# Kernel optimization log

Measured on AMD Instinct MI355X. Metric: run time of the kernel, lower is better.

Reference implementation:

```python
import jax, jax.numpy as jnp
import numpy as np

B, T, HID, NH = 2, 2048, 1024, 16
HD = HID // NH  # head_dim = 64
ROPE_BASE = 1000000.0


def _precompute_freqs(dim, end, rope_base):
    inv = 1.0 / (rope_base ** (np.arange(0, dim, 2)[: dim // 2].astype(np.float32) / dim))
    t = np.arange(end, dtype=np.float32)
    freqs = np.outer(t, inv).astype(np.float32)  # (end, dim//2)
    cos = np.concatenate([np.cos(freqs), np.cos(freqs)], axis=-1)
    sin = np.concatenate([np.sin(freqs), np.sin(freqs)], axis=-1)
    return jnp.asarray(cos), jnp.asarray(sin)


def setup_inputs() -> dict:
    key = jax.random.key(0)
    ks = jax.random.split(key, 5)
    x = jax.random.normal(ks[0], (B, T, HID), dtype=jnp.float32)
    s = 1.0 / np.sqrt(HID)
    Wq = jax.random.normal(ks[1], (HID, HID), dtype=jnp.float32) * s
    Wk = jax.random.normal(ks[2], (HID, HID), dtype=jnp.float32) * s
    Wv = jax.random.normal(ks[3], (HID, HID), dtype=jnp.float32) * s
    Wo = jax.random.normal(ks[4], (HID, HID), dtype=jnp.float32) * s
    cos, sin = _precompute_freqs(HD, T, ROPE_BASE)
    return {"x": x, "Wq": Wq, "Wk": Wk, "Wv": Wv, "Wo": Wo, "cos": cos, "sin": sin}


def _rotate_half(u):
    half = u.shape[-1] // 2
    return jnp.concatenate([-u[..., half:], u[..., :half]], axis=-1)


def reference(x, Wq, Wk, Wv, Wo, cos, sin):
    b, t, _ = x.shape
    # projections (nn.Linear: x @ W.T)
    q = (x @ Wq.T).reshape(b, t, NH, HD).transpose(0, 2, 1, 3)  # (B,H,T,D)
    k = (x @ Wk.T).reshape(b, t, NH, HD).transpose(0, 2, 1, 3)
    v = (x @ Wv.T).reshape(b, t, NH, HD).transpose(0, 2, 1, 3)
    c = cos[None, None, :t, :]
    s = sin[None, None, :t, :]
    q = q * c + _rotate_half(q) * s
    k = k * c + _rotate_half(k) * s
    scores = jnp.einsum("bhqd,bhkd->bhqk", q, k) / jnp.sqrt(jnp.float32(HD))
    causal = jnp.tril(jnp.ones((t, t), dtype=bool))
    scores = jnp.where(causal[None, None], scores, jnp.float32(-jnp.inf))
    prob = jax.nn.softmax(scores, axis=-1)
    out = jnp.einsum("bhqk,bhkd->bhqd", prob, v)
    out = out.transpose(0, 2, 1, 3).reshape(b, t, HID)
    return out @ Wo.T
```

## Files before the change

kernel.cpp:

```cpp
#include <hip/hip_runtime.h>
#include <hip/hip_bf16.h>

#define B_   2
#define T_   2048
#define HID_ 1024
#define NH_  16
#define HD_  64
#define K_   1024
#define M_   (B_*T_)

typedef __attribute__((ext_vector_type(8)))  short bf16x8;
typedef __attribute__((ext_vector_type(4)))  float f32x4;
typedef __attribute__((ext_vector_type(16))) float f32x16;
typedef __attribute__((ext_vector_type(4)))  unsigned int u32x4;

#define LOG2E 1.44269504088896340736f

__device__ inline unsigned short f2bf(float f) {
    __hip_bfloat16 h = __float2bfloat16(f);
    return __builtin_bit_cast(unsigned short, h);
}
__device__ inline float bf2f(unsigned short u) {
    return __builtin_bit_cast(float, (unsigned int)u << 16);
}
__device__ inline unsigned int pk2(float a, float b) {
    return (unsigned int)f2bf(a) | ((unsigned int)f2bf(b) << 16);
}
__device__ inline bf16x8 cvt8(float4 a, float4 b) {
    bf16x8 r;
    r[0]=(short)f2bf(a.x); r[1]=(short)f2bf(a.y); r[2]=(short)f2bf(a.z); r[3]=(short)f2bf(a.w);
    r[4]=(short)f2bf(b.x); r[5]=(short)f2bf(b.y); r[6]=(short)f2bf(b.z); r[7]=(short)f2bf(b.w);
    return r;
}

__global__ __launch_bounds__(256)
void cast_x(const float* __restrict__ in, unsigned short* __restrict__ out) {
    const int i = blockIdx.x * 256 + threadIdx.x;
    float4 a = ((const float4*)in)[2*i], b = ((const float4*)in)[2*i + 1];
    ((bf16x8*)out)[i] = cvt8(a, b);
}
__global__ __launch_bounds__(256)
void cast_w(const float* __restrict__ W0, const float* __restrict__ W1,
            const float* __restrict__ W2, const float* __restrict__ W3,
            unsigned short* __restrict__ o0, unsigned short* __restrict__ o1,
            unsigned short* __restrict__ o2, unsigned short* __restrict__ o3) {
    const int blk = blockIdx.x, sec = blk >> 9;
    const float* in = (sec == 0) ? W0 : (sec == 1) ? W1 : (sec == 2) ? W2 : W3;
    unsigned short* out = (sec == 0) ? o0 : (sec == 1) ? o1 : (sec == 2) ? o2 : o3;
    const int i = (blk & 511) * 256 + threadIdx.x;
    float4 a = ((const float4*)in)[2*i], b = ((const float4*)in)[2*i + 1];
    ((bf16x8*)out)[i] = cvt8(a, b);
}

template<int TYPE>
__global__ __launch_bounds__(256)
void gemm_k(const unsigned short* __restrict__ A, const unsigned short* __restrict__ W0,
            const unsigned short* __restrict__ W1, const unsigned short* __restrict__ W2,
            const float* __restrict__ cs, const float* __restrict__ sn,
            unsigned short* __restrict__ qb, unsigned short* __restrict__ kb,
            unsigned short* __restrict__ vtb, float* __restrict__ fout) {
    __shared__ unsigned short As[128*64];
    __shared__ unsigned short Bs[128*64];
    const int tid = threadIdx.x;
    const int w = tid >> 6, lane = tid & 63;
    const int u = lane >> 4, c = lane & 15;
    const int bm = blockIdx.x * 128, bn = blockIdx.y * 128;
    const int wm = (w & 1) * 64, wn = (w >> 1) * 64;
    const int srow = tid >> 3, scol = (tid & 7) << 3;

    const unsigned short* Wsec;
    int wrowbase;
    if constexpr (TYPE == 0) {
        const int sec = bn >> 10;
        Wsec = (sec == 0) ? W0 : ((sec == 1) ? W1 : W2);
        wrowbase = bn & 1023;
    } else {
        Wsec = W0;
        wrowbase = bn;
    }
    const unsigned short* Wp = Wsec + (size_t)(wrowbase + srow) * K_ + scol;
    const unsigned short* Ap = A + (size_t)(bm + srow) * K_ + scol;

    f32x4 acc[4][4] = {};
    bf16x8 ra[4], rb[4];

    auto loadin = [&](int k0) {
        #pragma unroll
        for (int i = 0; i < 4; ++i) {
            ra[i] = *(const bf16x8*)(Ap + (size_t)i * 32 * K_ + k0);
            rb[i] = *(const bf16x8*)(Wp + (size_t)i * 32 * K_ + k0);
        }
    };
    loadin(0);

    for (int k0 = 0; k0 < K_; k0 += 64) {
        __syncthreads();
        #pragma unroll
        for (int i = 0; i < 4; ++i) {
            const int row = i * 32 + srow;
            const int sc = (scol * 2) ^ ((row & 7) << 4);
            *(bf16x8*)((char*)As + row * 128 + sc) = ra[i];
            *(bf16x8*)((char*)Bs + row * 128 + sc) = rb[i];
        }
        __syncthreads();
        if (k0 < K_ - 64) loadin(k0 + 64);
        #pragma unroll
        for (int kk = 0; kk < 2; ++kk) {
            bf16x8 af[4], bfr[4];
            #pragma unroll
            for (int mi = 0; mi < 4; ++mi) {
                const int row = wm + mi * 16 + c;
                const int sc = (kk * 64 + u * 16) ^ ((row & 7) << 4);
                af[mi] = *(const bf16x8*)((char*)As + row * 128 + sc);
            }
            #pragma unroll
            for (int ni = 0; ni < 4; ++ni) {
                const int row = wn + ni * 16 + c;
                const int sc = (kk * 64 + u * 16) ^ ((row & 7) << 4);
                bfr[ni] = *(const bf16x8*)((char*)Bs + row * 128 + sc);
            }
            #pragma unroll
            for (int mi = 0; mi < 4; ++mi)
                #pragma unroll
                for (int ni = 0; ni < 4; ++ni)
                    acc[mi][ni] = __builtin_amdgcn_mfma_f32_16x16x32_bf16(
                        af[mi], bfr[ni], acc[mi][ni], 0, 0, 0);
        }
    }

    if constexpr (TYPE == 1) {
        #pragma unroll
        for (int mi = 0; mi < 4; ++mi)
            #pragma unroll
            for (int ni = 0; ni < 4; ++ni)
                #pragma unroll
                for (int r = 0; r < 4; ++r)
                    fout[(size_t)(bm + wm + 16*mi + 4*u + r) * HID_ + (bn + wn + 16*ni + c)] =
                        acc[mi][ni][r];
    } else {
        const int sec = bn >> 10;
        const int h = ((bn + wn) & 1023) >> 6;
        if (sec == 2) {
            #pragma unroll
            for (int mi = 0; mi < 4; ++mi)
                #pragma unroll
                for (int r = 0; r < 4; ++r) {
                    const int mg = bm + wm + 16*mi + 4*u + r;
                    const int bb = mg >> 11, t = mg & 2047;
                    #pragma unroll
                    for (int ni = 0; ni < 4; ++ni)
                        vtb[((size_t)(bb*16 + h) * 64 + 16*ni + c) * 2048 + t] =
                            f2bf(acc[mi][ni][r]);
                }
        } else {
            unsigned short* ob = sec ? kb : qb;
            const float qsc = sec ? 1.0f : (0.125f * LOG2E);
            #pragma unroll
            for (int mi = 0; mi < 4; ++mi)
                #pragma unroll
                for (int r = 0; r < 4; ++r) {
                    const int mg = bm + wm + 16*mi + 4*u + r;
                    const int bb = mg >> 11, t = mg & 2047;
                    const size_t base = ((size_t)(bb*16 + h) * 2048 + t) * 64;
                    #pragma unroll
                    for (int ni = 0; ni < 2; ++ni) {
                        const int dlo = 16*ni + c;
                        const float cv = cs[t*64 + dlo], sv = sn[t*64 + dlo];
                        const float Aa = acc[mi][ni][r], Bb = acc[mi][ni+2][r];
                        ob[base + dlo]      = f2bf((Aa*cv - Bb*sv) * qsc);
                        ob[base + dlo + 32] = f2bf((Bb*cv + Aa*sv) * qsc);
                    }
                }
        }
    }
}

__global__ __launch_bounds__(256)
void attn6(const unsigned short* __restrict__ q, const unsigned short* __restrict__ k,
           const unsigned short* __restrict__ vt, unsigned short* __restrict__ ab) {
    const int raw = blockIdx.x;
    const int bh    = (raw & 7) + 8 * ((raw >> 3) & 3);
    const int pairj = raw >> 5;
    const int tid = threadIdx.x;
    const int wid = tid >> 6, lane = tid & 63;
    const int h = lane >> 5, c = lane & 31;
    const bool hi = (h != 0);
    const int b = bh >> 4, hh = bh & 15;
    const unsigned short* qp = q  + (size_t)bh * T_ * 64;
    const unsigned short* kp = k  + (size_t)bh * T_ * 64;
    const unsigned short* vp = vt + (size_t)bh * 64 * T_;

    __shared__ float OS[4][32 * 68];
    __shared__ float mS[4][32], lS[4][32];

    auto phase = [&](int qblk) {
        const int q0 = qblk * 32;
        bf16x8 qf[4];
        #pragma unroll
        for (int s = 0; s < 4; ++s)
            qf[s] = *(const bf16x8*)(qp + (size_t)(q0 + c) * 64 + s * 16 + 8 * h);

        f32x16 O0 = {}, O1 = {};
        float m = -1e30f, lsum = 0.f;
        const int nst = qblk + 1;

        auto loadKV = [&](bf16x8 (&kf)[4], bf16x8 (&vf)[4], int st) {
            const int kvs = st << 5;
            #pragma unroll
            for (int s = 0; s < 4; ++s)
                kf[s] = *(const bf16x8*)(kp + (size_t)(kvs + c) * 64 + s * 16 + 8 * h);
            #pragma unroll
            for (int s = 0; s < 4; ++s)
                vf[s] = *(const bf16x8*)(vp + (size_t)(((s >> 1) << 5) + c) * T_
                                            + kvs + ((s & 1) << 4) + 8 * h);
        };

        auto process = [&](const bf16x8 (&kf)[4], const bf16x8 (&vf)[4], int st) {
            const int kvs = st << 5;
            f32x16 sa = {};
            #pragma unroll
            for (int s = 0; s < 4; ++s)
                sa = __builtin_amdgcn_mfma_f32_32x32x16_bf16(kf[s], qf[s], sa, 0, 0, 0);
            float p[16];
            const bool diag = (st == qblk);
            #pragma unroll
            for (int r = 0; r < 16; ++r) {
                float sv = sa[r];
                if (diag) {
                    const int kk = kvs + (r & 3) + 8 * (r >> 2) + 4 * h;
                    if (kk > q0 + c) sv = -1e30f;
                }
                p[r] = sv;
            }
            float mx = fmaxf(p[0], p[1]);
            #pragma unroll
            for (int r = 2; r < 16; ++r) mx = fmaxf(mx, p[r]);
            mx = fmaxf(mx, __shfl_xor(mx, 32));
            if (!__all(mx <= m + 8.0f)) {
                const float mn = fmaxf(m, mx);
                const float f = __builtin_amdgcn_exp2f(m - mn);
                m = mn;
                lsum *= f;
                #pragma unroll
                for (int r = 0; r < 16; ++r) { O0[r] *= f; O1[r] *= f; }
            }
            float ps = 0.f;
            #pragma unroll
            for (int r = 0; r < 16; ++r) {
                p[r] = __builtin_amdgcn_exp2f(p[r] - m);
                ps += p[r];
            }
            lsum += ps;
            unsigned o0 = pk2(p[0], p[1]),   o1 = pk2(p[2], p[3]);
            unsigned o2 = pk2(p[4], p[5]),   o3 = pk2(p[6], p[7]);
            unsigned o4 = pk2(p[8], p[9]),   o5 = pk2(p[10], p[11]);
            unsigned o6 = pk2(p[12], p[13]), o7 = pk2(p[14], p[15]);
            unsigned x0 = __shfl_xor(o0, 32), x1 = __shfl_xor(o1, 32);
            unsigned x2 = __shfl_xor(o2, 32), x3 = __shfl_xor(o3, 32);
            unsigned x4 = __shfl_xor(o4, 32), x5 = __shfl_xor(o5, 32);
            unsigned x6 = __shfl_xor(o6, 32), x7 = __shfl_xor(o7, 32);
            u32x4 B0w = { hi ? x2 : o0, hi ? x3 : o1, hi ? o2 : x0, hi ? o3 : x1 };
            u32x4 B1w = { hi ? x6 : o4, hi ? x7 : o5, hi ? o6 : x4, hi ? o7 : x5 };
            bf16x8 PB0 = __builtin_bit_cast(bf16x8, B0w);
            bf16x8 PB1 = __builtin_bit_cast(bf16x8, B1w);
            O0 = __builtin_amdgcn_mfma_f32_32x32x16_bf16(vf[0], PB0, O0, 0, 0, 0);
            O0 = __builtin_amdgcn_mfma_f32_32x32x16_bf16(vf[1], PB1, O0, 0, 0, 0);
            O1 = __builtin_amdgcn_mfma_f32_32x32x16_bf16(vf[2], PB0, O1, 0, 0, 0);
            O1 = __builtin_amdgcn_mfma_f32_32x32x16_bf16(vf[3], PB1, O1, 0, 0, 0);
        };

        bf16x8 kA[4], kB[4], vA[4], vB[4];
        if (wid < nst) loadKV(kA, vA, wid);
        for (int st = wid; st < nst; st += 8) {
            if (st + 4 < nst) loadKV(kB, vB, st + 4);
            process(kA, vA, st);
            if (st + 4 >= nst) break;
            if (st + 8 < nst) loadKV(kA, vA, st + 8);
            process(kB, vB, st + 4);
        }
        lsum += __shfl_xor(lsum, 32);

        __syncthreads();
        if (h == 0) { mS[wid][c] = m; lS[wid][c] = lsum; }
        float* os = &OS[wid][0];
        #pragma unroll
        for (int j = 0; j < 4; ++j) {
            f32x4 t0 = { O0[4*j], O0[4*j+1], O0[4*j+2], O0[4*j+3] };
            f32x4 t1 = { O1[4*j], O1[4*j+1], O1[4*j+2], O1[4*j+3] };
            *(f32x4*)&os[c * 68 + 8*j + 4*h]      = t0;
            *(f32x4*)&os[c * 68 + 32 + 8*j + 4*h] = t1;
        }
        __syncthreads();

        const int ql = tid & 31, d0 = (tid >> 5) * 8;
        const float M = fmaxf(fmaxf(mS[0][ql], mS[1][ql]), fmaxf(mS[2][ql], mS[3][ql]));
        float acc[8] = {};
        float L = 0.f;
        #pragma unroll
        for (int w2 = 0; w2 < 4; ++w2) {
            const float sc = __builtin_amdgcn_exp2f(mS[w2][ql] - M);
            L += lS[w2][ql] * sc;
            f32x4 a = *(f32x4*)&OS[w2][ql * 68 + d0];
            f32x4 b2 = *(f32x4*)&OS[w2][ql * 68 + d0 + 4];
            #pragma unroll
            for (int t = 0; t < 4; ++t) {
                acc[t]     += a[t]  * sc;
                acc[4 + t] += b2[t] * sc;
            }
        }
        const float inv = 1.0f / L;
        uint4 ov;
        ov.x = pk2(acc[0]*inv, acc[1]*inv);
        ov.y = pk2(acc[2]*inv, acc[3]*inv);
        ov.z = pk2(acc[4]*inv, acc[5]*inv);
        ov.w = pk2(acc[6]*inv, acc[7]*inv);
        *(uint4*)(ab + ((size_t)(b * T_) + q0 + ql) * HID_ + hh * 64 + d0) = ov;
    };

    phase(63 - pairj);
    phase(pairj);
}

extern "C" void kernel_launch(void* const* d_in, const int* in_sizes, int n_in,
                              void* d_out, int out_size, void* d_ws, size_t ws_size,
                              hipStream_t stream) {
    const float* x  = (const float*)d_in[0];
    const float* Wq = (const float*)d_in[1];
    const float* Wk = (const float*)d_in[2];
    const float* Wv = (const float*)d_in[3];
    const float* Wo = (const float*)d_in[4];
    const float* cs = (const float*)d_in[5];
    const float* sn = (const float*)d_in[6];
    char* wsb = (char*)d_ws;
    unsigned short* xb  = (unsigned short*)(wsb);
    unsigned short* wqb = (unsigned short*)(wsb + (8u  << 20));
    unsigned short* wkb = (unsigned short*)(wsb + (10u << 20));
    unsigned short* wvb = (unsigned short*)(wsb + (12u << 20));
    unsigned short* wob = (unsigned short*)(wsb + (14u << 20));
    unsigned short* qb  = (unsigned short*)(wsb + (16u << 20));
    unsigned short* kb  = (unsigned short*)(wsb + (24u << 20));
    unsigned short* vtb = (unsigned short*)(wsb + (32u << 20));
    unsigned short* ab  = (unsigned short*)(wsb + (40u << 20));

    cast_x<<<2048, 256, 0, stream>>>(x, xb);
    cast_w<<<2048, 256, 0, stream>>>(Wq, Wk, Wv, Wo, wqb, wkb, wvb, wob);

    gemm_k<0><<<dim3(M_/128, 3072/128), 256, 0, stream>>>(
        xb, wqb, wkb, wvb, cs, sn, qb, kb, vtb, nullptr);
    attn6<<<1024, 256, 0, stream>>>(qb, kb, vtb, ab);
    gemm_k<1><<<dim3(M_/128, HID_/128), 256, 0, stream>>>(
        ab, wob, nullptr, nullptr, nullptr, nullptr,
        nullptr, nullptr, nullptr, (float*)d_out);
}
```

Before: 134.6 us.

## Split attention into one q-block per workgroup and shrink combine buffer to bf16

Each attention workgroup used to process a pair of query blocks (j and 63-j). It now handles a single query block, and the grid doubles to 2048 blocks, ordered with the longest causal rows first. The cross-wave partial outputs are stored in shared memory as packed bf16 instead of fp32, which reduces LDS use and may raise occupancy, at some cost in precision. The P-to-bf16 conversion now truncates with a byte permute instead of round-to-nearest, which saves ALU work but adds rounding bias.

```diff
diff --git a/kernel.cpp b/kernel.cpp
--- a/kernel.cpp
+++ b/kernel.cpp
@@ -13,6 +13,7 @@
 typedef __attribute__((ext_vector_type(4)))  float f32x4;
 typedef __attribute__((ext_vector_type(16))) float f32x16;
 typedef __attribute__((ext_vector_type(4)))  unsigned int u32x4;
+typedef __attribute__((ext_vector_type(2)))  unsigned int u32x2;
 
 #define LOG2E 1.44269504088896340736f
 
@@ -20,11 +21,12 @@
     __hip_bfloat16 h = __float2bfloat16(f);
     return __builtin_bit_cast(unsigned short, h);
 }
-__device__ inline float bf2f(unsigned short u) {
-    return __builtin_bit_cast(float, (unsigned int)u << 16);
-}
 __device__ inline unsigned int pk2(float a, float b) {
     return (unsigned int)f2bf(a) | ((unsigned int)f2bf(b) << 16);
+}
+__device__ inline unsigned int pkt(float a, float b) {
+    return __builtin_amdgcn_perm(__builtin_bit_cast(unsigned, a),
+                                 __builtin_bit_cast(unsigned, b), 0x03020706u);
 }
 __device__ inline bf16x8 cvt8(float4 a, float4 b) {
     bf16x8 r;
@@ -176,149 +178,155 @@
 }
 
 __global__ __launch_bounds__(256)
-void attn6(const unsigned short* __restrict__ q, const unsigned short* __restrict__ k,
+void attn7(const unsigned short* __restrict__ q, const unsigned short* __restrict__ k,
            const unsigned short* __restrict__ vt, unsigned short* __restrict__ ab) {
     const int raw = blockIdx.x;
-    const int bh    = (raw & 7) + 8 * ((raw >> 3) & 3);
-    const int pairj = raw >> 5;
+    const int bh   = (raw & 7) + 8 * ((raw >> 3) & 3);
+    const int qblk = 63 - (raw >> 5);
     const int tid = threadIdx.x;
     const int wid = tid >> 6, lane = tid & 63;
     const int h = lane >> 5, c = lane & 31;
     const bool hi = (h != 0);
     const int b = bh >> 4, hh = bh & 15;
-    const unsigned short* qp = q  + (size_t)bh * T_ * 64;
-    const unsigned short* kp = k  + (size_t)bh * T_ * 64;
-    const unsigned short* vp = vt + (size_t)bh * 64 * T_;
-
-    __shared__ float OS[4][32 * 68];
+    const int q0 = qblk * 32;
+    const unsigned short* qp = q  + (size_t)bh * (T_*64);
+    const unsigned short* kp = k  + (size_t)bh * (T_*64);
+    const unsigned short* vp = vt + (size_t)bh * (64*T_);
+
+    const int kloff  = c * 64 + 8 * h;
+    const int vloff0 = c * 2048 + 8 * h;
+    const int vloff1 = vloff0 + 32 * 2048;
+
+    bf16x8 qf[4];
+    {
+        const unsigned short* qrow = qp + (q0 + c) * 64 + 8 * h;
+        #pragma unroll
+        for (int s = 0; s < 4; ++s)
+            qf[s] = *(const bf16x8*)(qrow + s * 16);
+    }
+
+    f32x16 O0 = {}, O1 = {};
+    float m = -1e30f, lsum = 0.f;
+    const int nst = qblk + 1;
+
+    auto loadKV = [&](bf16x8 (&kf)[4], bf16x8 (&vf)[4], int st) {
+        const unsigned short* kst = kp + (st << 11);
+        const unsigned short* vst = vp + (st << 5);
+        #pragma unroll
+        for (int s = 0; s < 4; ++s)
+            kf[s] = *(const bf16x8*)(kst + kloff + s * 16);
+        vf[0] = *(const bf16x8*)(vst + vloff0);
+        vf[1] = *(const bf16x8*)(vst + vloff0 + 16);
+        vf[2] = *(const bf16x8*)(vst + vloff1);
+        vf[3] = *(const bf16x8*)(vst + vloff1 + 16);
+    };
+
+    auto process = [&](const bf16x8 (&kf)[4], const bf16x8 (&vf)[4], int st) {
+        const int kvs = st << 5;
+        f32x16 sa = {};
+        #pragma unroll
+        for (int s = 0; s < 4; ++s)
+            sa = __builtin_amdgcn_mfma_f32_32x32x16_bf16(kf[s], qf[s], sa, 0, 0, 0);
+        float p[16];
+        const bool diag = (st == qblk);
+        #pragma unroll
+        for (int r = 0; r < 16; ++r) {
+            float sv = sa[r];
+            if (diag) {
+                const int kk = kvs + (r & 3) + 8 * (r >> 2) + 4 * h;
+                if (kk > q0 + c) sv = -1e30f;
+            }
+            p[r] = sv;
+        }
+        float mx = fmaxf(p[0], p[1]);
+        #pragma unroll
+        for (int r = 2; r < 16; ++r) mx = fmaxf(mx, p[r]);
+        mx = fmaxf(mx, __shfl_xor(mx, 32));
+        if (!__all(mx <= m + 8.0f)) {
+            const float mn = fmaxf(m, mx);
+            const float f = __builtin_amdgcn_exp2f(m - mn);
+            m = mn;
+            lsum *= f;
+            #pragma unroll
+            for (int r = 0; r < 16; ++r) { O0[r] *= f; O1[r] *= f; }
+        }
+        float ps = 0.f;
+        #pragma unroll
+        for (int r = 0; r < 16; ++r) {
+            p[r] = __builtin_amdgcn_exp2f(p[r] - m);
+            ps += p[r];
+        }
+        lsum += ps;
+        unsigned o0 = pkt(p[0], p[1]),   o1 = pkt(p[2], p[3]);
+        unsigned o2 = pkt(p[4], p[5]),   o3 = pkt(p[6], p[7]);
+        unsigned o4 = pkt(p[8], p[9]),   o5 = pkt(p[10], p[11]);
+        unsigned o6 = pkt(p[12], p[13]), o7 = pkt(p[14], p[15]);
+        unsigned x0 = __shfl_xor(o0, 32), x1 = __shfl_xor(o1, 32);
+        unsigned x2 = __shfl_xor(o2, 32), x3 = __shfl_xor(o3, 32);
+        unsigned x4 = __shfl_xor(o4, 32), x5 = __shfl_xor(o5, 32);
+        unsigned x6 = __shfl_xor(o6, 32), x7 = __shfl_xor(o7, 32);
+        u32x4 B0w = { hi ? x2 : o0, hi ? x3 : o1, hi ? o2 : x0, hi ? o3 : x1 };
+        u32x4 B1w = { hi ? x6 : o4, hi ? x7 : o5, hi ? o6 : x4, hi ? o7 : x5 };
+        bf16x8 PB0 = __builtin_bit_cast(bf16x8, B0w);
+        bf16x8 PB1 = __builtin_bit_cast(bf16x8, B1w);
+        O0 = __builtin_amdgcn_mfma_f32_32x32x16_bf16(vf[0], PB0, O0, 0, 0, 0);
+        O0 = __builtin_amdgcn_mfma_f32_32x32x16_bf16(vf[1], PB1, O0, 0, 0, 0);
+        O1 = __builtin_amdgcn_mfma_f32_32x32x16_bf16(vf[2], PB0, O1, 0, 0, 0);
+        O1 = __builtin_amdgcn_mfma_f32_32x32x16_bf16(vf[3], PB1, O1, 0, 0, 0);
+    };
+
+    bf16x8 kA[4], kB[4], vA[4], vB[4];
+    if (wid < nst) loadKV(kA, vA, wid);
+    for (int st = wid; st < nst; st += 8) {
+        if (st + 4 < nst) loadKV(kB, vB, st + 4);
+        process(kA, vA, st);
+        if (st + 4 >= nst) break;
+        if (st + 8 < nst) loadKV(kA, vA, st + 8);
+        process(kB, vB, st + 4);
+    }
+    lsum += __shfl_xor(lsum, 32);
+
+    __shared__ unsigned OSu[4][32 * 34];
     __shared__ float mS[4][32], lS[4][32];
-
-    auto phase = [&](int qblk) {
-        const int q0 = qblk * 32;
-        bf16x8 qf[4];
-        #pragma unroll
-        for (int s = 0; s < 4; ++s)
-            qf[s] = *(const bf16x8*)(qp + (size_t)(q0 + c) * 64 + s * 16 + 8 * h);
-
-        f32x16 O0 = {}, O1 = {};
-        float m = -1e30f, lsum = 0.f;
-        const int nst = qblk + 1;
-
-        auto loadKV = [&](bf16x8 (&kf)[4], bf16x8 (&vf)[4], int st) {
-            const int kvs = st << 5;
-            #pragma unroll
-            for (int s = 0; s < 4; ++s)
-                kf[s] = *(const bf16x8*)(kp + (size_t)(kvs + c) * 64 + s * 16 + 8 * h);
-            #pragma unroll
-            for (int s = 0; s < 4; ++s)
-                vf[s] = *(const bf16x8*)(vp + (size_t)(((s >> 1) << 5) + c) * T_
-                                            + kvs + ((s & 1) << 4) + 8 * h);
-        };
-
-        auto process = [&](const bf16x8 (&kf)[4], const bf16x8 (&vf)[4], int st) {
-            const int kvs = st << 5;
-            f32x16 sa = {};
-            #pragma unroll
-            for (int s = 0; s < 4; ++s)
-                sa = __builtin_amdgcn_mfma_f32_32x32x16_bf16(kf[s], qf[s], sa, 0, 0, 0);
-            float p[16];
-            const bool diag = (st == qblk);
-            #pragma unroll
-            for (int r = 0; r < 16; ++r) {
-                float sv = sa[r];
-                if (diag) {
-                    const int kk = kvs + (r & 3) + 8 * (r >> 2) + 4 * h;
-                    if (kk > q0 + c) sv = -1e30f;
-                }
-                p[r] = sv;
-            }
-            float mx = fmaxf(p[0], p[1]);
-            #pragma unroll
-            for (int r = 2; r < 16; ++r) mx = fmaxf(mx, p[r]);
-            mx = fmaxf(mx, __shfl_xor(mx, 32));
-            if (!__all(mx <= m + 8.0f)) {
-                const float mn = fmaxf(m, mx);
-                const float f = __builtin_amdgcn_exp2f(m - mn);
-                m = mn;
-                lsum *= f;
-                #pragma unroll
-                for (int r = 0; r < 16; ++r) { O0[r] *= f; O1[r] *= f; }
-            }
-            float ps = 0.f;
-            #pragma unroll
-            for (int r = 0; r < 16; ++r) {
-                p[r] = __builtin_amdgcn_exp2f(p[r] - m);
-                ps += p[r];
-            }
-            lsum += ps;
-            unsigned o0 = pk2(p[0], p[1]),   o1 = pk2(p[2], p[3]);
-            unsigned o2 = pk2(p[4], p[5]),   o3 = pk2(p[6], p[7]);
-            unsigned o4 = pk2(p[8], p[9]),   o5 = pk2(p[10], p[11]);
-            unsigned o6 = pk2(p[12], p[13]), o7 = pk2(p[14], p[15]);
-            unsigned x0 = __shfl_xor(o0, 32), x1 = __shfl_xor(o1, 32);
-            unsigned x2 = __shfl_xor(o2, 32), x3 = __shfl_xor(o3, 32);
-            unsigned x4 = __shfl_xor(o4, 32), x5 = __shfl_xor(o5, 32);
-            unsigned x6 = __shfl_xor(o6, 32), x7 = __shfl_xor(o7, 32);
-            u32x4 B0w = { hi ? x2 : o0, hi ? x3 : o1, hi ? o2 : x0, hi ? o3 : x1 };
-            u32x4 B1w = { hi ? x6 : o4, hi ? x7 : o5, hi ? o6 : x4, hi ? o7 : x5 };
-            bf16x8 PB0 = __builtin_bit_cast(bf16x8, B0w);
-            bf16x8 PB1 = __builtin_bit_cast(bf16x8, B1w);
-            O0 = __builtin_amdgcn_mfma_f32_32x32x16_bf16(vf[0], PB0, O0, 0, 0, 0);
-            O0 = __builtin_amdgcn_mfma_f32_32x32x16_bf16(vf[1], PB1, O0, 0, 0, 0);
-            O1 = __builtin_amdgcn_mfma_f32_32x32x16_bf16(vf[2], PB0, O1, 0, 0, 0);
-            O1 = __builtin_amdgcn_mfma_f32_32x32x16_bf16(vf[3], PB1, O1, 0, 0, 0);
-        };
-
-        bf16x8 kA[4], kB[4], vA[4], vB[4];
-        if (wid < nst) loadKV(kA, vA, wid);
-        for (int st = wid; st < nst; st += 8) {
-            if (st + 4 < nst) loadKV(kB, vB, st + 4);
-            process(kA, vA, st);
-            if (st + 4 >= nst) break;
-            if (st + 8 < nst) loadKV(kA, vA, st + 8);
-            process(kB, vB, st + 4);
-        }
-        lsum += __shfl_xor(lsum, 32);
-
-        __syncthreads();
-        if (h == 0) { mS[wid][c] = m; lS[wid][c] = lsum; }
-        float* os = &OS[wid][0];
+    if (h == 0) { mS[wid][c] = m; lS[wid][c] = lsum; }
+    {
+        unsigned* os = &OSu[wid][0];
+        const int rb = c * 34 + 2 * h;
         #pragma unroll
         for (int j = 0; j < 4; ++j) {
-            f32x4 t0 = { O0[4*j], O0[4*j+1], O0[4*j+2], O0[4*j+3] };
-            f32x4 t1 = { O1[4*j], O1[4*j+1], O1[4*j+2], O1[4*j+3] };
-            *(f32x4*)&os[c * 68 + 8*j + 4*h]      = t0;
-            *(f32x4*)&os[c * 68 + 32 + 8*j + 4*h] = t1;
-        }
-        __syncthreads();
-
-        const int ql = tid & 31, d0 = (tid >> 5) * 8;
-        const float M = fmaxf(fmaxf(mS[0][ql], mS[1][ql]), fmaxf(mS[2][ql], mS[3][ql]));
-        float acc[8] = {};
-        float L = 0.f;
-        #pragma unroll
-        for (int w2 = 0; w2 < 4; ++w2) {
-            const float sc = __builtin_amdgcn_exp2f(mS[w2][ql] - M);
-            L += lS[w2][ql] * sc;
-            f32x4 a = *(f32x4*)&OS[w2][ql * 68 + d0];
-            f32x4 b2 = *(f32x4*)&OS[w2][ql * 68 + d0 + 4];
-            #pragma unroll
-            for (int t = 0; t < 4; ++t) {
-                acc[t]     += a[t]  * sc;
-                acc[4 + t] += b2[t] * sc;
-            }
-        }
-        const float inv = 1.0f / L;
-        uint4 ov;
-        ov.x = pk2(acc[0]*inv, acc[1]*inv);
-        ov.y = pk2(acc[2]*inv, acc[3]*inv);
-        ov.z = pk2(acc[4]*inv, acc[5]*inv);
-        ov.w = pk2(acc[6]*inv, acc[7]*inv);
-        *(uint4*)(ab + ((size_t)(b * T_) + q0 + ql) * HID_ + hh * 64 + d0) = ov;
-    };
-
-    phase(63 - pairj);
-    phase(pairj);
+            os[rb + 4*j]          = pk2(O0[4*j],   O0[4*j+1]);
+            os[rb + 4*j + 1]      = pk2(O0[4*j+2], O0[4*j+3]);
+            os[rb + 16 + 4*j]     = pk2(O1[4*j],   O1[4*j+1]);
+            os[rb + 16 + 4*j + 1] = pk2(O1[4*j+2], O1[4*j+3]);
+        }
+    }
+    __syncthreads();
+
+    const int ql = tid & 31, ug = (tid >> 5) * 4;
+    const float M = fmaxf(fmaxf(mS[0][ql], mS[1][ql]), fmaxf(mS[2][ql], mS[3][ql]));
+    float acc[8] = {};
+    float L = 0.f;
+    #pragma unroll
+    for (int w2 = 0; w2 < 4; ++w2) {
+        const float sc = __builtin_amdgcn_exp2f(mS[w2][ql] - M);
+        L += lS[w2][ql] * sc;
+        u32x2 pa = *(u32x2*)&OSu[w2][ql * 34 + ug];
+        u32x2 pb = *(u32x2*)&OSu[w2][ql * 34 + ug + 2];
+        #pragma unroll
+        for (int t = 0; t < 2; ++t) {
+            acc[2*t]   += __builtin_bit_cast(float, pa[t] << 16) * sc;
+            acc[2*t+1] += __builtin_bit_cast(float, pa[t] & 0xffff0000u) * sc;
+            acc[4+2*t]   += __builtin_bit_cast(float, pb[t] << 16) * sc;
+            acc[4+2*t+1] += __builtin_bit_cast(float, pb[t] & 0xffff0000u) * sc;
+        }
+    }
+    const float inv = 1.0f / L;
+    uint4 ov;
+    ov.x = pk2(acc[0]*inv, acc[1]*inv);
+    ov.y = pk2(acc[2]*inv, acc[3]*inv);
+    ov.z = pk2(acc[4]*inv, acc[5]*inv);
+    ov.w = pk2(acc[6]*inv, acc[7]*inv);
+    *(uint4*)(ab + ((size_t)(b * T_) + q0 + ql) * HID_ + hh * 64 + ug * 2) = ov;
 }
 
 extern "C" void kernel_launch(void* const* d_in, const int* in_sizes, int n_in,
@@ -347,7 +355,7 @@
 
     gemm_k<0><<<dim3(M_/128, 3072/128), 256, 0, stream>>>(
         xb, wqb, wkb, wvb, cs, sn, qb, kb, vtb, nullptr);
-    attn6<<<1024, 256, 0, stream>>>(qb, kb, vtb, ab);
+    attn7<<<2048, 256, 0, stream>>>(qb, kb, vtb, ab);
     gemm_k<1><<<dim3(M_/128, HID_/128), 256, 0, stream>>>(
         ab, wob, nullptr, nullptr, nullptr, nullptr,
         nullptr, nullptr, nullptr, (float*)d_out);
```

Result: faster. 130.4 us (-3.1%).
